# Optimization experiments

Hardware: AMD Instinct MI355X
Metric: run time of the kernel (lower is better)

Reference implementation:

```python
import jax, jax.numpy as jnp
import numpy as np

B = 8192; L = 50; D_EMB = 128
N_USER = 100000; N_MOVIE = 50000; N_DENSE = 8
D = 2 * D_EMB + D_EMB + N_DENSE  # 392 total_input_dim
E = 4; T = 2; H1 = 256; H2 = 128; ATT_H = 64; N_CROSS = 3


def setup_inputs() -> dict:
    key = jax.random.key(0)
    ks = jax.random.split(key, 28)
    rn = lambda k, shape, s=0.02: jax.random.normal(k, shape, jnp.float32) * s
    inp = {
        'userId': jax.random.randint(ks[0], (B,), 0, N_USER),
        'movieId': jax.random.randint(ks[1], (B,), 0, N_MOVIE),
        'seq_history': jax.random.randint(ks[2], (B, L), 0, N_MOVIE),
        'dense_feats': jax.random.normal(ks[3], (B, N_DENSE), jnp.float32),
        # embeddings (row 0 is padding_idx -> zeros)
        'emb_user': rn(ks[4], (N_USER + 1, D_EMB)).at[0].set(0.0),
        'emb_movie': rn(ks[5], (N_MOVIE + 1, D_EMB)).at[0].set(0.0),
        # DIN attention MLP: input [q,k,q-k,q*k] = 4*D_EMB
        'att_w1': rn(ks[6], (4 * D_EMB, ATT_H)), 'att_b1': jnp.zeros((ATT_H,), jnp.float32),
        'att_w2': rn(ks[7], (ATT_H, 1)), 'att_b2': jnp.zeros((1,), jnp.float32),
        # LayerNorms
        'in_gamma': jnp.ones((D,), jnp.float32), 'in_beta': jnp.zeros((D,), jnp.float32),
        'cr_gamma': jnp.ones((D,), jnp.float32), 'cr_beta': jnp.zeros((D,), jnp.float32),
        # CrossNetV2: x_{l+1} = x0 * (x_l W_l + b_l) + x_l
        'cross_W': rn(ks[8], (N_CROSS, D, D)), 'cross_b': jnp.zeros((N_CROSS, D), jnp.float32),
        # MMoE experts: Linear(D,H1)-ReLU-Linear(H1,H2), batched over E
        'exp_w1': rn(ks[9], (E, D, H1)), 'exp_b1': jnp.zeros((E, H1), jnp.float32),
        'exp_w2': rn(ks[10], (E, H1, H2)), 'exp_b2': jnp.zeros((E, H2), jnp.float32),
        # gates per task
        'gate_w': rn(ks[11], (T, D, E)), 'gate_b': jnp.zeros((T, E), jnp.float32),
        # task heads Linear(H2, 1)
        'head_w': rn(ks[12], (T, H2)), 'head_b': jnp.zeros((T,), jnp.float32),
    }
    return inp


def _layernorm(x, g, b, eps=1e-5):
    m = jnp.mean(x, axis=-1, keepdims=True)
    v = jnp.var(x, axis=-1, keepdims=True)
    return (x - m) * jax.lax.rsqrt(v + eps) * g + b


def _forward(userId, movieId, seq_history, dense_feats, emb_user, emb_movie,
             att_w1, att_b1, att_w2, att_b2, in_gamma, in_beta,
             cross_W, cross_b, cr_gamma, cr_beta,
             exp_w1, exp_b1, exp_w2, exp_b2, gate_w, gate_b, head_w, head_b):
    # sparse embedding gathers
    user_e = emb_user[userId]            # [B, D_EMB]
    movie_e = emb_movie[movieId]         # [B, D_EMB]  (target item)
    hist = emb_movie[seq_history]        # [B, L, D_EMB]
    mask = seq_history > 0               # [B, L]

    # DIN attention pooling
    q = jnp.broadcast_to(movie_e[:, None, :], hist.shape)            # [B, L, D_EMB]
    att_in = jnp.concatenate([q, hist, q - hist, q * hist], axis=-1)  # [B, L, 4*D_EMB]
    scores = (jax.nn.relu(att_in @ att_w1 + att_b1) @ att_w2 + att_b2)[..., 0]  # [B, L]
    scores = jnp.where(mask, scores, -1e9)
    probs = jax.nn.softmax(scores, axis=-1)                           # [B, L]
    interest = jnp.einsum('bl,bld->bd', probs, hist)                  # [B, D_EMB]

    x = jnp.concatenate([user_e, movie_e, interest, dense_feats], axis=-1)  # [B, D]
    x = _layernorm(x, in_gamma, in_beta)

    # CrossNetV2
    x0 = x
    for l in range(N_CROSS):
        x = x0 * (x @ cross_W[l] + cross_b[l]) + x
    x = _layernorm(x, cr_gamma, cr_beta)

    # MMoE: batched expert GEMMs + per-task soft gates
    h = jax.nn.relu(jnp.einsum('bd,edh->ebh', x, exp_w1) + exp_b1[:, None, :])  # [E,B,H1]
    eo = jnp.einsum('ebh,eho->ebo', h, exp_w2) + exp_b2[:, None, :]             # [E,B,H2]
    g = jax.nn.softmax(jnp.einsum('bd,tde->tbe', x, gate_w) + gate_b[:, None, :], axis=-1)  # [T,B,E]
    task_feat = jnp.einsum('tbe,ebo->tbo', g, eo)                                # [T,B,H2]

    logits = jnp.einsum('tbo,to->tb', task_feat, head_w) + head_b[:, None]       # [T,B]
    return logits


def reference(userId, movieId, seq_history, dense_feats, emb_user, emb_movie,
              att_w1, att_b1, att_w2, att_b2, in_gamma, in_beta,
              cross_W, cross_b, cr_gamma, cr_beta,
              exp_w1, exp_b1, exp_w2, exp_b2, gate_w, gate_b, head_w, head_b):
    return _forward(userId, movieId, seq_history, dense_feats, emb_user, emb_movie,
                    att_w1, att_b1, att_w2, att_b2, in_gamma, in_beta,
                    cross_W, cross_b, cr_gamma, cr_beta,
                    exp_w1, exp_b1, exp_w2, exp_b2, gate_w, gate_b, head_w, head_b)
```

## Files before the change

kernel.cpp:

```cpp
#include <hip/hip_runtime.h>
#include <hip/hip_bf16.h>

typedef short short8 __attribute__((ext_vector_type(8)));
typedef short short4v __attribute__((ext_vector_type(4)));
typedef float f32x4 __attribute__((ext_vector_type(4)));

constexpr int BB = 8192;
constexpr int LL = 50;
constexpr int DE = 128;
constexpr int DD = 392;
constexpr int HH1 = 256;
constexpr int HH2 = 128;

__device__ __forceinline__ short f2b(float x) {
    __hip_bfloat16 h = __float2bfloat16(x);
    return __builtin_bit_cast(short, h);
}
__device__ __forceinline__ float b2f(short v) {
    unsigned u = ((unsigned)(unsigned short)v) << 16;
    return __builtin_bit_cast(float, u);
}

__global__ __launch_bounds__(256) void prep_small(
    const float* __restrict__ w1,
    const float* __restrict__ w2, const float* __restrict__ b2,
    const float* __restrict__ head_w,
    short* __restrict__ WqpT, float* __restrict__ WkpFf,
    float* __restrict__ hw2, float* __restrict__ hc)
{
    __shared__ float hw[256];
    const int b = blockIdx.x, t = threadIdx.x;
    if (b < 32) {
        int o = b * 256 + t;
        int h = o >> 7, d = o & 127;
        WqpT[o] = f2b(w1[d * 64 + h] + w1[16384 + d * 64 + h]);
    } else if (b < 64) {
        int o = (b - 32) * 256 + t;
        int e = o & 7, lane = (o >> 3) & 63, nt = (o >> 9) & 3, kt = o >> 11;
        int k = (kt << 5) + ((lane >> 4) << 3) + e;
        int h = (nt << 4) + (lane & 15);
        int base = (o >> 3) << 4;
        WkpFf[base + e]     = w1[(128 + k) * 64 + h] - w1[(256 + k) * 64 + h];
        WkpFf[base + 8 + e] = w1[(384 + k) * 64 + h];
    } else {
        const int e = b - 64;
        hw[t] = head_w[t];
        __syncthreads();
        const float* row = &w2[((long)e * HH1 + t) * HH2];
        float s0 = 0.f, s1 = 0.f;
        #pragma unroll 8
        for (int o = 0; o < 128; o += 4) {
            float4 v = *reinterpret_cast<const float4*>(&row[o]);
            s0 += v.x * hw[o] + v.y * hw[o + 1] + v.z * hw[o + 2] + v.w * hw[o + 3];
            s1 += v.x * hw[128 + o] + v.y * hw[129 + o] + v.z * hw[130 + o] + v.w * hw[131 + o];
        }
        hw2[(((e << 8) + t) << 1) + 0] = s0;
        hw2[(((e << 8) + t) << 1) + 1] = s1;
        if (t < 2) {
            float s = 0.f;
            for (int o = 0; o < 128; ++o) s += b2[e * 128 + o] * hw[t * 128 + o];
            hc[e * 2 + t] = s;
        }
    }
}

constexpr int S0 = 3 * 392 * 392;
constexpr int S1 = 4 * 392 * 256;
constexpr int S2 = (50001 * 128) / 4;
constexpr int S3 = (BB * 128) / 4;

__global__ __launch_bounds__(256) void prep_trans(
    const float* __restrict__ cross_W, const float* __restrict__ exp_w1,
    const float* __restrict__ emb_movie, const int* __restrict__ movieId,
    short* __restrict__ WTc, short* __restrict__ WT1, short* __restrict__ embB,
    short* __restrict__ qb)
{
    int idx = blockIdx.x * 256 + threadIdx.x;
    if (idx < S0) {
        int z = idx / (392 * 392), rr = idx - z * 392 * 392;
        int c = rr / 392, r = rr - c * 392;
        WTc[idx] = f2b(cross_W[(long)z * 153664 + r * 392 + c]);
    } else if (idx < S0 + S1) {
        int j = idx - S0;
        int z = j / 100352, rr = j - z * 100352;
        int c = rr / 392, r = rr - c * 392;
        WT1[j] = f2b(exp_w1[(long)z * 100352 + r * 256 + c]);
    } else if (idx < S0 + S1 + S2) {
        long j = (long)(idx - S0 - S1) << 2;
        float4 v = *reinterpret_cast<const float4*>(&emb_movie[j]);
        short4v o;
        o[0] = f2b(v.x); o[1] = f2b(v.y); o[2] = f2b(v.z); o[3] = f2b(v.w);
        *reinterpret_cast<short4v*>(&embB[j]) = o;
    } else if (idx < S0 + S1 + S2 + S3) {
        int j = idx - S0 - S1 - S2;
        int bb = j >> 5, d0 = (j & 31) << 2;
        float4 v = *reinterpret_cast<const float4*>(
            &emb_movie[(long)movieId[bb] * DE + d0]);
        short4v o;
        o[0] = f2b(v.x); o[1] = f2b(v.y); o[2] = f2b(v.z); o[3] = f2b(v.w);
        *reinterpret_cast<short4v*>(&qb[bb * DE + d0]) = o;
    }
}

__global__ __launch_bounds__(256, 8) void attn_kernel(
    const int* __restrict__ userId, const int* __restrict__ movieId,
    const int* __restrict__ seq, const float* __restrict__ dense,
    const float* __restrict__ emb_user, const float* __restrict__ emb_movie,
    const short* __restrict__ embB,
    const float* __restrict__ qcAll, const float* __restrict__ WkpFf,
    const float* __restrict__ att_w2, const float* __restrict__ att_b2,
    const float* __restrict__ in_gamma, const float* __restrict__ in_beta,
    float* __restrict__ x0f, short* __restrict__ x0b)
{
    __shared__ short hist[64 * 128];
    __shared__ float qs[128];
    __shared__ int   seq_s[64];
    __shared__ float spS[4][64];
    __shared__ float probs[64];
    __shared__ float ibuf[4][128];
    __shared__ float stats[2];

    const int b = blockIdx.x;
    const int t = threadIdx.x;
    const int lane = t & 63;
    const int w = t >> 6;

    if (t < 128) qs[t] = emb_movie[(long)movieId[b] * DE + t];
    if (t < 64)  seq_s[t] = (t < LL) ? seq[b * LL + t] : 0;
    __syncthreads();

    #pragma unroll
    for (int i = 0; i < 4; ++i) {
        const int idx = t + (i << 8);
        const int l = idx >> 4, c = idx & 15;
        short8 hv = *reinterpret_cast<const short8*>(&embB[(long)seq_s[l] * DE + (c << 3)]);
        const int byte = (l << 8) + ((c << 4) ^ ((l & 7) << 4));
        *reinterpret_cast<short8*>(reinterpret_cast<char*>(hist) + byte) = hv;
    }

    const int col = (w << 4) + (lane & 15);
    float ue = (t < 128) ? emb_user[(long)userId[b] * DE + t] : 0.f;
    float dv = (t >= 128 && t < 136) ? dense[b * 8 + (t - 128)] : 0.f;
    const float qc  = qcAll[((long)b << 6) + col];
    const float w2v = att_w2[col];

    short8 bfrag[4];
    #pragma unroll
    for (int kt = 0; kt < 4; ++kt) {
        const float* wkp = &WkpFf[((((kt << 2) + w) << 6) | lane) << 4];
        const int kq = (kt << 5) + ((lane >> 4) << 3);
        #pragma unroll
        for (int j = 0; j < 8; ++j)
            bfrag[kt][j] = f2b(fmaf(qs[kq + j], wkp[8 + j], wkp[j]));
    }
    __syncthreads();

    #pragma unroll
    for (int mt = 0; mt < 4; ++mt) {
        f32x4 acc = {0.f, 0.f, 0.f, 0.f};
        const int row = (mt << 4) + (lane & 15);
        const int rbase = row << 8;
        const int swz = (row & 7) << 4;
        #pragma unroll
        for (int kt = 0; kt < 4; ++kt) {
            const int kbyte = (kt << 6) + ((lane >> 4) << 4);
            short8 a = *reinterpret_cast<const short8*>(
                reinterpret_cast<char*>(hist) + rbase + (kbyte ^ swz));
            acc = __builtin_amdgcn_mfma_f32_16x16x32_bf16(a, bfrag[kt], acc, 0, 0, 0);
        }
        #pragma unroll
        for (int r = 0; r < 4; ++r) {
            float v = fmaxf(acc[r] + qc, 0.f) * w2v;
            v += __shfl_xor(v, 1); v += __shfl_xor(v, 2);
            v += __shfl_xor(v, 4); v += __shfl_xor(v, 8);
            if ((lane & 15) == 0)
                spS[w][(mt << 4) + ((lane >> 4) << 2) + r] = v;
        }
    }
    __syncthreads();

    if (t < 64) {
        float sc = spS[0][t] + spS[1][t] + spS[2][t] + spS[3][t] + att_b2[0];
        float s = (t < LL) ? ((seq_s[t] > 0) ? sc : -1e9f) : -INFINITY;
        float m = s;
        #pragma unroll
        for (int off = 32; off > 0; off >>= 1) m = fmaxf(m, __shfl_xor(m, off));
        float e = (t < LL) ? __expf(s - m) : 0.f;
        float sum = e;
        #pragma unroll
        for (int off = 32; off > 0; off >>= 1) sum += __shfl_xor(sum, off);
        probs[t] = (t < LL) ? (e / sum) : 0.f;
    }
    __syncthreads();

    const int g  = t >> 5;
    const int d0 = (t & 31) << 2;
    float4 ps = make_float4(0.f, 0.f, 0.f, 0.f);
    #pragma unroll
    for (int i = 0; i < 8; ++i) {
        const int l = g + (i << 3);
        const int byte = (l << 8) + ((d0 << 1) ^ ((l & 7) << 4));
        short4v hv = *reinterpret_cast<const short4v*>(
            reinterpret_cast<const char*>(hist) + byte);
        const float p = probs[l];
        ps.x = fmaf(p, b2f(hv[0]), ps.x);
        ps.y = fmaf(p, b2f(hv[1]), ps.y);
        ps.z = fmaf(p, b2f(hv[2]), ps.z);
        ps.w = fmaf(p, b2f(hv[3]), ps.w);
    }
    ps.x += __shfl_xor(ps.x, 32); ps.y += __shfl_xor(ps.y, 32);
    ps.z += __shfl_xor(ps.z, 32); ps.w += __shfl_xor(ps.w, 32);
    if (lane < 32)
        *reinterpret_cast<float4*>(&ibuf[w][lane << 2]) = ps;
    __syncthreads();

    float v0 = (t < 128) ? ue : qs[t - 128];
    float v1 = 0.f;
    if (t < 128)       v1 = ibuf[0][t] + ibuf[1][t] + ibuf[2][t] + ibuf[3][t];
    else if (t < 136)  v1 = dv;

    float s2 = v0 + v1, q2 = v0 * v0 + v1 * v1;
    #pragma unroll
    for (int off = 32; off > 0; off >>= 1) {
        s2 += __shfl_xor(s2, off);
        q2 += __shfl_xor(q2, off);
    }
    if (lane == 0) { spS[0][w] = s2; spS[1][w] = q2; }
    __syncthreads();
    if (t == 0) {
        float S = spS[0][0] + spS[0][1] + spS[0][2] + spS[0][3];
        float Q = spS[1][0] + spS[1][1] + spS[1][2] + spS[1][3];
        float mean = S / (float)DD;
        float var = Q / (float)DD - mean * mean;
        stats[0] = mean;
        stats[1] = rsqrtf(var + 1e-5f);
    }
    __syncthreads();
    const float mean = stats[0], inv = stats[1];
    const long base = (long)b * DD;
    float o0 = (v0 - mean) * inv * in_gamma[t] + in_beta[t];
    x0f[base + t] = o0; x0b[base + t] = f2b(o0);
    if (t < 136) {
        float o1 = (v1 - mean) * inv * in_gamma[256 + t] + in_beta[256 + t];
        x0f[base + 256 + t] = o1; x0b[base + 256 + t] = f2b(o1);
    }
}

template<int MODE, int WF32, int WB16, int NXB, int NZB>
__global__ __launch_bounds__(256) void bgemm(
    const short* __restrict__ A, const short* __restrict__ WT,
    const float* __restrict__ bias,
    float* __restrict__ outF, short* __restrict__ outB,
    const float* __restrict__ x0, const float* __restrict__ xin,
    int M, int N, int K, long aZ, long wZ, long bZ, long oZ)
{
    __shared__ short As[2][64 * 64];
    __shared__ short Bs[2][64 * 64];

    int id = blockIdx.x;
    const int qq = (int)gridDim.x >> 3;
    id = (id & 7) * qq + (id >> 3);
    const int mb  = id / (NXB * NZB);
    const int rem = id - mb * (NXB * NZB);
    const int z   = rem / NXB;
    const int xb  = rem - z * NXB;

    A += (long)z * aZ; WT += (long)z * wZ; bias += (long)z * bZ;
    const long oz = (long)z * oZ;

    const int t = threadIdx.x, w = t >> 6, lane = t & 63;
    const int m0 = mb * 64, n0 = xb * 64;
    const int sm = t >> 3, sk8 = (t & 7) << 3;

    f32x4 acc[4];
    #pragma unroll
    for (int i = 0; i < 4; ++i) {
        #pragma unroll
        for (int r = 0; r < 4; ++r) acc[i][r] = 0.f;
    }

    const int nsteps = (K + 63) >> 6;
    short8 avA[2], bvA[2], avB[2], bvB[2];

    auto loadA = [&](int k0) {
        #pragma unroll
        for (int i = 0; i < 2; ++i) {
            const int r = sm + (i << 5);
            short8 zv = {0, 0, 0, 0, 0, 0, 0, 0};
            avA[i] = zv; bvA[i] = zv;
            if (k0 + sk8 < K) {
                avA[i] = *reinterpret_cast<const short8*>(&A[(long)(m0 + r) * K + k0 + sk8]);
                if (n0 + r < N)
                    bvA[i] = *reinterpret_cast<const short8*>(&WT[(long)(n0 + r) * K + k0 + sk8]);
            }
        }
    };
    auto loadB = [&](int k0) {
        #pragma unroll
        for (int i = 0; i < 2; ++i) {
            const int r = sm + (i << 5);
            short8 zv = {0, 0, 0, 0, 0, 0, 0, 0};
            avB[i] = zv; bvB[i] = zv;
            if (k0 + sk8 < K) {
                avB[i] = *reinterpret_cast<const short8*>(&A[(long)(m0 + r) * K + k0 + sk8]);
                if (n0 + r < N)
                    bvB[i] = *reinterpret_cast<const short8*>(&WT[(long)(n0 + r) * K + k0 + sk8]);
            }
        }
    };
    auto wrA = [&](int buf) {
        #pragma unroll
        for (int i = 0; i < 2; ++i) {
            const int r = sm + (i << 5);
            const int byte = (r << 7) + ((sk8 << 1) ^ ((r & 7) << 4));
            *reinterpret_cast<short8*>(reinterpret_cast<char*>(&As[buf][0]) + byte) = avA[i];
            *reinterpret_cast<short8*>(reinterpret_cast<char*>(&Bs[buf][0]) + byte) = bvA[i];
        }
    };
    auto wrB = [&](int buf) {
        #pragma unroll
        for (int i = 0; i < 2; ++i) {
            const int r = sm + (i << 5);
            const int byte = (r << 7) + ((sk8 << 1) ^ ((r & 7) << 4));
            *reinterpret_cast<short8*>(reinterpret_cast<char*>(&As[buf][0]) + byte) = avB[i];
            *reinterpret_cast<short8*>(reinterpret_cast<char*>(&Bs[buf][0]) + byte) = bvB[i];
        }
    };
    auto domfma = [&](int buf) {
        #pragma unroll
        for (int kt = 0; kt < 2; ++kt) {
            const int kbyte = (kt << 6) + ((lane >> 4) << 4);
            const int ar = (w << 4) + (lane & 15);
            short8 a = *reinterpret_cast<const short8*>(
                reinterpret_cast<char*>(&As[buf][0]) + (ar << 7) + (kbyte ^ ((ar & 7) << 4)));
            #pragma unroll
            for (int nt = 0; nt < 4; ++nt) {
                const int br = (nt << 4) + (lane & 15);
                short8 bb = *reinterpret_cast<const short8*>(
                    reinterpret_cast<char*>(&Bs[buf][0]) + (br << 7) + (kbyte ^ ((br & 7) << 4)));
                acc[nt] = __builtin_amdgcn_mfma_f32_16x16x32_bf16(a, bb, acc[nt], 0, 0, 0);
            }
        }
    };

    loadA(0);
    wrA(0);
    if (nsteps > 1) loadA(64);
    if (nsteps > 2) loadB(128);
    __syncthreads();

    int cur = 0, s = 0;
    while (s + 1 < nsteps) {
        domfma(cur);
        wrA(cur ^ 1);
        if (s + 3 < nsteps) loadA((s + 3) << 6);
        __syncthreads(); cur ^= 1; ++s;
        if (s + 1 < nsteps) {
            domfma(cur);
            wrB(cur ^ 1);
            if (s + 3 < nsteps) loadB((s + 3) << 6);
            __syncthreads(); cur ^= 1; ++s;
        }
    }
    domfma(cur);

    #pragma unroll
    for (int nt = 0; nt < 4; ++nt) {
        const int col = n0 + (nt << 4) + (lane & 15);
        if (col < N) {
            const float bv = bias[col];
            #pragma unroll
            for (int r = 0; r < 4; ++r) {
                const int row = m0 + (w << 4) + ((lane >> 4) << 2) + r;
                float v = acc[nt][r] + bv;
                if (MODE == 1) v = fmaxf(v, 0.f);
                const long o = (long)row * N + col;
                if (MODE == 2) v = x0[o] * v + xin[o];
                if (WF32) outF[oz + o] = v;
                if (WB16) outB[oz + o] = f2b(v);
            }
        }
    }
}

__global__ __launch_bounds__(256) void ln_kernel(
    const float* __restrict__ in,
    const float* __restrict__ gamma, const float* __restrict__ beta,
    float* __restrict__ outF, short* __restrict__ outB)
{
    __shared__ float red[2][4];
    __shared__ float stats[2];
    const int b = blockIdx.x, t = threadIdx.x, lane = t & 63, w = t >> 6;
    const long base = (long)b * DD;
    float v0 = in[base + t];
    float v1 = (t < 136) ? in[base + 256 + t] : 0.f;
    float s = v0 + v1, q2 = v0 * v0 + v1 * v1;
    #pragma unroll
    for (int off = 32; off > 0; off >>= 1) {
        s += __shfl_xor(s, off);
        q2 += __shfl_xor(q2, off);
    }
    if (lane == 0) { red[0][w] = s; red[1][w] = q2; }
    __syncthreads();
    if (t == 0) {
        float S = red[0][0] + red[0][1] + red[0][2] + red[0][3];
        float Q = red[1][0] + red[1][1] + red[1][2] + red[1][3];
        float mean = S / (float)DD;
        float var = Q / (float)DD - mean * mean;
        stats[0] = mean;
        stats[1] = rsqrtf(var + 1e-5f);
    }
    __syncthreads();
    const float mean = stats[0], inv = stats[1];
    float o0 = (v0 - mean) * inv * gamma[t] + beta[t];
    outF[base + t] = o0; outB[base + t] = f2b(o0);
    if (t < 136) {
        float o1 = (v1 - mean) * inv * gamma[256 + t] + beta[256 + t];
        outF[base + 256 + t] = o1; outB[base + 256 + t] = f2b(o1);
    }
}

__global__ __launch_bounds__(256) void final_kernel(
    const float* __restrict__ x, const short* __restrict__ h1,
    const float* __restrict__ hw2, const float* __restrict__ hc,
    const float* __restrict__ gate_w, const float* __restrict__ gate_b,
    const float* __restrict__ head_b, float* __restrict__ out)
{
    const int t = threadIdx.x, lane = t & 63, w = t >> 6;
    const int b = blockIdx.x * 4 + w;
    const float* xr = x + (long)b * DD;

    float xv[7];
    #pragma unroll
    for (int i = 0; i < 7; ++i) {
        int d = lane + (i << 6);
        xv[i] = (d < DD) ? xr[d] : 0.f;
    }

    float gl[8] = {0.f, 0.f, 0.f, 0.f, 0.f, 0.f, 0.f, 0.f};
    #pragma unroll
    for (int i = 0; i < 7; ++i) {
        int d = lane + (i << 6);
        if (d < DD) {
            float4 g0 = *reinterpret_cast<const float4*>(&gate_w[d << 2]);
            float4 g1 = *reinterpret_cast<const float4*>(&gate_w[1568 + (d << 2)]);
            gl[0] = fmaf(xv[i], g0.x, gl[0]); gl[1] = fmaf(xv[i], g0.y, gl[1]);
            gl[2] = fmaf(xv[i], g0.z, gl[2]); gl[3] = fmaf(xv[i], g0.w, gl[3]);
            gl[4] = fmaf(xv[i], g1.x, gl[4]); gl[5] = fmaf(xv[i], g1.y, gl[5]);
            gl[6] = fmaf(xv[i], g1.z, gl[6]); gl[7] = fmaf(xv[i], g1.w, gl[7]);
        }
    }

    float ed[8];
    #pragma unroll
    for (int e = 0; e < 4; ++e) {
        short4v hv = *reinterpret_cast<const short4v*>(
            &h1[((long)e * BB + b) * HH1 + (lane << 2)]);
        const float* hwp = &hw2[(((e << 8) + (lane << 2))) << 1];
        float4 w01 = *reinterpret_cast<const float4*>(hwp);
        float4 w23 = *reinterpret_cast<const float4*>(hwp + 4);
        float h0 = b2f(hv[0]), h1f = b2f(hv[1]), h2 = b2f(hv[2]), h3 = b2f(hv[3]);
        ed[e]     = fmaf(h0, w01.x, fmaf(h1f, w01.z, fmaf(h2, w23.x, h3 * w23.z)));
        ed[4 + e] = fmaf(h0, w01.y, fmaf(h1f, w01.w, fmaf(h2, w23.y, h3 * w23.w)));
    }

    #pragma unroll
    for (int v = 0; v < 8; ++v) {
        #pragma unroll
        for (int off = 32; off > 0; off >>= 1) {
            gl[v] += __shfl_xor(gl[v], off);
            ed[v] += __shfl_xor(ed[v], off);
        }
    }

    if (lane == 0) {
        float res[2];
        #pragma unroll
        for (int tt = 0; tt < 2; ++tt) {
            float lv[4], m = -1e30f;
            #pragma unroll
            for (int e = 0; e < 4; ++e) {
                lv[e] = gl[tt * 4 + e] + gate_b[tt * 4 + e];
                m = fmaxf(m, lv[e]);
            }
            float sum = 0.f, acc = 0.f;
            #pragma unroll
            for (int e = 0; e < 4; ++e) { lv[e] = __expf(lv[e] - m); sum += lv[e]; }
            #pragma unroll
            for (int e = 0; e < 4; ++e)
                acc = fmaf(lv[e], ed[tt * 4 + e] + hc[e * 2 + tt], acc);
            res[tt] = head_b[tt] + acc / sum;
        }
        out[b] = res[0];
        out[BB + b] = res[1];
    }
}

extern "C" void kernel_launch(void* const* d_in, const int* in_sizes, int n_in,
                              void* d_out, int out_size, void* d_ws, size_t ws_size,
                              hipStream_t stream) {
    const int*   userId    = (const int*)d_in[0];
    const int*   movieId   = (const int*)d_in[1];
    const int*   seq       = (const int*)d_in[2];
    const float* dense     = (const float*)d_in[3];
    const float* emb_user  = (const float*)d_in[4];
    const float* emb_movie = (const float*)d_in[5];
    const float* att_w1    = (const float*)d_in[6];
    const float* att_b1    = (const float*)d_in[7];
    const float* att_w2    = (const float*)d_in[8];
    const float* att_b2    = (const float*)d_in[9];
    const float* in_gamma  = (const float*)d_in[10];
    const float* in_beta   = (const float*)d_in[11];
    const float* cr_gamma  = (const float*)d_in[12];
    const float* cr_beta   = (const float*)d_in[13];
    const float* cross_W   = (const float*)d_in[14];
    const float* cross_b   = (const float*)d_in[15];
    const float* exp_w1    = (const float*)d_in[16];
    const float* exp_b1    = (const float*)d_in[17];
    const float* exp_w2    = (const float*)d_in[18];
    const float* exp_b2    = (const float*)d_in[19];
    const float* gate_w    = (const float*)d_in[20];
    const float* gate_b    = (const float*)d_in[21];
    const float* head_w    = (const float*)d_in[22];
    const float* head_b    = (const float*)d_in[23];
    float* outp = (float*)d_out;

    char* p = (char*)d_ws;
    auto alloc = [&](size_t bytes) -> char* {
        char* r = p; p += (bytes + 255) & ~(size_t)255; return r;
    };
    short* WqpT  = (short*)alloc(8192 * 2);
    float* WkpFf = (float*)alloc(16384 * 4);
    float* hw2 = (float*)alloc(2048 * 4);
    float* hc  = (float*)alloc(8 * 4);
    short* WTc = (short*)alloc((size_t)3 * 392 * 392 * 2);
    short* WT1 = (short*)alloc((size_t)4 * 256 * 392 * 2);
    short* embB = (short*)alloc((size_t)50001 * 128 * 2);
    short* qb   = (short*)alloc((size_t)BB * DE * 2);
    float* qcAll = (float*)alloc((size_t)BB * 64 * 4);
    float* x0f = (float*)alloc((size_t)BB * DD * 4);
    short* x0b = (short*)alloc((size_t)BB * DD * 2);
    float* xAf = (float*)alloc((size_t)BB * DD * 4);
    short* xAb = (short*)alloc((size_t)BB * DD * 2);
    float* xBf = (float*)alloc((size_t)BB * DD * 4);
    short* xBb = (short*)alloc((size_t)BB * DD * 2);
    short* h1b = (short*)alloc((size_t)4 * BB * HH1 * 2);

    prep_small<<<68, 256, 0, stream>>>(att_w1, exp_w2, exp_b2, head_w,
                                       WqpT, WkpFf, hw2, hc);
    prep_trans<<<(S0 + S1 + S2 + S3 + 255) / 256, 256, 0, stream>>>(
        cross_W, exp_w1, emb_movie, movieId, WTc, WT1, embB, qb);

    bgemm<0, 1, 0, 1, 1><<<128, 256, 0, stream>>>(
        qb, WqpT, att_b1, qcAll, nullptr, nullptr, nullptr,
        BB, 64, DE, 0, 0, 0, 0);

    attn_kernel<<<BB, 256, 0, stream>>>(userId, movieId, seq, dense,
                                        emb_user, emb_movie, embB,
                                        qcAll, WkpFf,
                                        att_w2, att_b2,
                                        in_gamma, in_beta, x0f, x0b);

    bgemm<2, 1, 1, 7, 1><<<896, 256, 0, stream>>>(x0b, WTc, cross_b, xAf, xAb,
                                                  x0f, x0f, BB, DD, DD, 0, 0, 0, 0);
    bgemm<2, 1, 1, 7, 1><<<896, 256, 0, stream>>>(xAb, WTc + 392 * 392, cross_b + 392,
                                                  xBf, xBb, x0f, xAf, BB, DD, DD, 0, 0, 0, 0);
    bgemm<2, 1, 0, 7, 1><<<896, 256, 0, stream>>>(xBb, WTc + 2 * 392 * 392, cross_b + 784,
                                                  xAf, nullptr, x0f, xBf, BB, DD, DD, 0, 0, 0, 0);

    ln_kernel<<<BB, 256, 0, stream>>>(xAf, cr_gamma, cr_beta, xBf, xBb);

    bgemm<1, 0, 1, 4, 4><<<2048, 256, 0, stream>>>(
        xBb, WT1, exp_b1, nullptr, h1b, nullptr, nullptr,
        BB, HH1, DD, 0, (long)HH1 * DD, HH1, (long)BB * HH1);

    final_kernel<<<BB / 4, 256, 0, stream>>>(xBf, h1b, hw2, hc,
                                             gate_w, gate_b, head_b, outp);

    (void)in_sizes; (void)n_in; (void)out_size; (void)ws_size;
}
```

Before: 177.2 us.

## Merge prep kernels, compute query projection inline, simplify GEMM pipeline, drop fp32 LN output

Folds the two prep kernels and the small query-projection GEMM into one prep_all launch, which computes qcAll directly from emb_movie rows with scalar FMAs. This removes two launches and the qb and WqpT intermediates. The GEMM main loop goes from a two-deep register prefetch to a single-buffer prefetch, which cuts register pressure but may hide less load latency. The layernorm now writes only bf16, and the final kernel reads bf16 x for the gate logits, which halves traffic there at some cost in precision.

```diff
diff --git a/kernel.cpp b/kernel.cpp
--- a/kernel.cpp
+++ b/kernel.cpp
@@ -21,29 +21,37 @@
     return __builtin_bit_cast(float, u);
 }
 
-__global__ __launch_bounds__(256) void prep_small(
+constexpr int S0 = 3 * 392 * 392;
+constexpr int S1 = 4 * 392 * 256;
+constexpr int S2 = (50001 * 128) / 4;
+constexpr int NB_TRANS = 9619;
+constexpr int QC0 = 36 + NB_TRANS;
+constexpr int NB_PREP = QC0 + 2048;
+
+__global__ __launch_bounds__(256) void prep_all(
     const float* __restrict__ w1,
     const float* __restrict__ w2, const float* __restrict__ b2,
-    const float* __restrict__ head_w,
-    short* __restrict__ WqpT, float* __restrict__ WkpFf,
-    float* __restrict__ hw2, float* __restrict__ hc)
+    const float* __restrict__ head_w, const float* __restrict__ att_b1,
+    const float* __restrict__ cross_W, const float* __restrict__ exp_w1,
+    const float* __restrict__ emb_movie, const int* __restrict__ movieId,
+    float* __restrict__ WkpFf, float* __restrict__ hw2, float* __restrict__ hc,
+    short* __restrict__ WTc, short* __restrict__ WT1, short* __restrict__ embB,
+    float* __restrict__ qcAll)
 {
-    __shared__ float hw[256];
-    const int b = blockIdx.x, t = threadIdx.x;
-    if (b < 32) {
-        int o = b * 256 + t;
-        int h = o >> 7, d = o & 127;
-        WqpT[o] = f2b(w1[d * 64 + h] + w1[16384 + d * 64 + h]);
-    } else if (b < 64) {
-        int o = (b - 32) * 256 + t;
+    __shared__ float sh[4][128];
+    const int blk = blockIdx.x, t = threadIdx.x;
+
+    if (blk < 32) {
+        int o = blk * 256 + t;
         int e = o & 7, lane = (o >> 3) & 63, nt = (o >> 9) & 3, kt = o >> 11;
         int k = (kt << 5) + ((lane >> 4) << 3) + e;
         int h = (nt << 4) + (lane & 15);
         int base = (o >> 3) << 4;
         WkpFf[base + e]     = w1[(128 + k) * 64 + h] - w1[(256 + k) * 64 + h];
         WkpFf[base + 8 + e] = w1[(384 + k) * 64 + h];
-    } else {
-        const int e = b - 64;
+    } else if (blk < 36) {
+        const int e = blk - 32;
+        float* hw = &sh[0][0];
         hw[t] = head_w[t];
         __syncthreads();
         const float* row = &w2[((long)e * HH1 + t) * HH2];
@@ -61,44 +69,37 @@
             for (int o = 0; o < 128; ++o) s += b2[e * 128 + o] * hw[t * 128 + o];
             hc[e * 2 + t] = s;
         }
-    }
-}
-
-constexpr int S0 = 3 * 392 * 392;
-constexpr int S1 = 4 * 392 * 256;
-constexpr int S2 = (50001 * 128) / 4;
-constexpr int S3 = (BB * 128) / 4;
-
-__global__ __launch_bounds__(256) void prep_trans(
-    const float* __restrict__ cross_W, const float* __restrict__ exp_w1,
-    const float* __restrict__ emb_movie, const int* __restrict__ movieId,
-    short* __restrict__ WTc, short* __restrict__ WT1, short* __restrict__ embB,
-    short* __restrict__ qb)
-{
-    int idx = blockIdx.x * 256 + threadIdx.x;
-    if (idx < S0) {
-        int z = idx / (392 * 392), rr = idx - z * 392 * 392;
-        int c = rr / 392, r = rr - c * 392;
-        WTc[idx] = f2b(cross_W[(long)z * 153664 + r * 392 + c]);
-    } else if (idx < S0 + S1) {
-        int j = idx - S0;
-        int z = j / 100352, rr = j - z * 100352;
-        int c = rr / 392, r = rr - c * 392;
-        WT1[j] = f2b(exp_w1[(long)z * 100352 + r * 256 + c]);
-    } else if (idx < S0 + S1 + S2) {
-        long j = (long)(idx - S0 - S1) << 2;
-        float4 v = *reinterpret_cast<const float4*>(&emb_movie[j]);
-        short4v o;
-        o[0] = f2b(v.x); o[1] = f2b(v.y); o[2] = f2b(v.z); o[3] = f2b(v.w);
-        *reinterpret_cast<short4v*>(&embB[j]) = o;
-    } else if (idx < S0 + S1 + S2 + S3) {
-        int j = idx - S0 - S1 - S2;
-        int bb = j >> 5, d0 = (j & 31) << 2;
-        float4 v = *reinterpret_cast<const float4*>(
-            &emb_movie[(long)movieId[bb] * DE + d0]);
-        short4v o;
-        o[0] = f2b(v.x); o[1] = f2b(v.y); o[2] = f2b(v.z); o[3] = f2b(v.w);
-        *reinterpret_cast<short4v*>(&qb[bb * DE + d0]) = o;
+    } else if (blk < QC0) {
+        int idx = (blk - 36) * 256 + t;
+        if (idx < S0) {
+            int z = idx / (392 * 392), rr = idx - z * 392 * 392;
+            int c = rr / 392, r = rr - c * 392;
+            WTc[idx] = f2b(cross_W[(long)z * 153664 + r * 392 + c]);
+        } else if (idx < S0 + S1) {
+            int j = idx - S0;
+            int z = j / 100352, rr = j - z * 100352;
+            int c = rr / 392, r = rr - c * 392;
+            WT1[j] = f2b(exp_w1[(long)z * 100352 + r * 256 + c]);
+        } else if (idx < S0 + S1 + S2) {
+            long j = (long)(idx - S0 - S1) << 2;
+            float4 v = *reinterpret_cast<const float4*>(&emb_movie[j]);
+            short4v o;
+            o[0] = f2b(v.x); o[1] = f2b(v.y); o[2] = f2b(v.z); o[3] = f2b(v.w);
+            *reinterpret_cast<short4v*>(&embB[j]) = o;
+        }
+    } else {
+        const int w = t >> 6, lane = t & 63;
+        const int b = (blk - QC0) * 4 + w;
+        if (lane < 32)
+            *reinterpret_cast<float4*>(&sh[w][lane << 2]) =
+                *reinterpret_cast<const float4*>(
+                    &emb_movie[(long)movieId[b] * DE + (lane << 2)]);
+        __syncthreads();
+        float s = att_b1[lane];
+        #pragma unroll 8
+        for (int d = 0; d < 128; ++d)
+            s = fmaf(sh[w][d], w1[d * 64 + lane] + w1[16384 + d * 64 + lane], s);
+        qcAll[((long)b << 6) + lane] = s;
     }
 }
 
@@ -211,7 +212,7 @@
     ps.x += __shfl_xor(ps.x, 32); ps.y += __shfl_xor(ps.y, 32);
     ps.z += __shfl_xor(ps.z, 32); ps.w += __shfl_xor(ps.w, 32);
     if (lane < 32)
-        *reinterpret_cast<float4*>(&ibuf[w][lane << 2]) = ps;
+        *reinterpret_cast<float4*>(&ibuf[w][(lane & 31) << 2]) = ps;
     __syncthreads();
 
     float v0 = (t < 128) ? ue : qs[t - 128];
@@ -280,7 +281,7 @@
     }
 
     const int nsteps = (K + 63) >> 6;
-    short8 avA[2], bvA[2], avB[2], bvB[2];
+    short8 avA[2], bvA[2];
 
     auto loadA = [&](int k0) {
         #pragma unroll
@@ -295,19 +296,6 @@
             }
         }
     };
-    auto loadB = [&](int k0) {
-        #pragma unroll
-        for (int i = 0; i < 2; ++i) {
-            const int r = sm + (i << 5);
-            short8 zv = {0, 0, 0, 0, 0, 0, 0, 0};
-            avB[i] = zv; bvB[i] = zv;
-            if (k0 + sk8 < K) {
-                avB[i] = *reinterpret_cast<const short8*>(&A[(long)(m0 + r) * K + k0 + sk8]);
-                if (n0 + r < N)
-                    bvB[i] = *reinterpret_cast<const short8*>(&WT[(long)(n0 + r) * K + k0 + sk8]);
-            }
-        }
-    };
     auto wrA = [&](int buf) {
         #pragma unroll
         for (int i = 0; i < 2; ++i) {
@@ -315,15 +303,6 @@
             const int byte = (r << 7) + ((sk8 << 1) ^ ((r & 7) << 4));
             *reinterpret_cast<short8*>(reinterpret_cast<char*>(&As[buf][0]) + byte) = avA[i];
             *reinterpret_cast<short8*>(reinterpret_cast<char*>(&Bs[buf][0]) + byte) = bvA[i];
-        }
-    };
-    auto wrB = [&](int buf) {
-        #pragma unroll
-        for (int i = 0; i < 2; ++i) {
-            const int r = sm + (i << 5);
-            const int byte = (r << 7) + ((sk8 << 1) ^ ((r & 7) << 4));
-            *reinterpret_cast<short8*>(reinterpret_cast<char*>(&As[buf][0]) + byte) = avB[i];
-            *reinterpret_cast<short8*>(reinterpret_cast<char*>(&Bs[buf][0]) + byte) = bvB[i];
         }
     };
     auto domfma = [&](int buf) {
@@ -346,21 +325,15 @@
     loadA(0);
     wrA(0);
     if (nsteps > 1) loadA(64);
-    if (nsteps > 2) loadB(128);
-    __syncthreads();
-
-    int cur = 0, s = 0;
-    while (s + 1 < nsteps) {
+    __syncthreads();
+
+    int cur = 0;
+    for (int s = 0; s + 1 < nsteps; ++s) {
         domfma(cur);
         wrA(cur ^ 1);
-        if (s + 3 < nsteps) loadA((s + 3) << 6);
-        __syncthreads(); cur ^= 1; ++s;
-        if (s + 1 < nsteps) {
-            domfma(cur);
-            wrB(cur ^ 1);
-            if (s + 3 < nsteps) loadB((s + 3) << 6);
-            __syncthreads(); cur ^= 1; ++s;
-        }
+        if (s + 2 < nsteps) loadA((s + 2) << 6);
+        __syncthreads();
+        cur ^= 1;
     }
     domfma(cur);
 
@@ -386,7 +359,7 @@
 __global__ __launch_bounds__(256) void ln_kernel(
     const float* __restrict__ in,
     const float* __restrict__ gamma, const float* __restrict__ beta,
-    float* __restrict__ outF, short* __restrict__ outB)
+    short* __restrict__ outB)
 {
     __shared__ float red[2][4];
     __shared__ float stats[2];
@@ -412,29 +385,26 @@
     }
     __syncthreads();
     const float mean = stats[0], inv = stats[1];
-    float o0 = (v0 - mean) * inv * gamma[t] + beta[t];
-    outF[base + t] = o0; outB[base + t] = f2b(o0);
-    if (t < 136) {
-        float o1 = (v1 - mean) * inv * gamma[256 + t] + beta[256 + t];
-        outF[base + 256 + t] = o1; outB[base + 256 + t] = f2b(o1);
-    }
+    outB[base + t] = f2b((v0 - mean) * inv * gamma[t] + beta[t]);
+    if (t < 136)
+        outB[base + 256 + t] = f2b((v1 - mean) * inv * gamma[256 + t] + beta[256 + t]);
 }
 
 __global__ __launch_bounds__(256) void final_kernel(
-    const float* __restrict__ x, const short* __restrict__ h1,
+    const short* __restrict__ x, const short* __restrict__ h1,
     const float* __restrict__ hw2, const float* __restrict__ hc,
     const float* __restrict__ gate_w, const float* __restrict__ gate_b,
     const float* __restrict__ head_b, float* __restrict__ out)
 {
     const int t = threadIdx.x, lane = t & 63, w = t >> 6;
     const int b = blockIdx.x * 4 + w;
-    const float* xr = x + (long)b * DD;
+    const short* xr = x + (long)b * DD;
 
     float xv[7];
     #pragma unroll
     for (int i = 0; i < 7; ++i) {
         int d = lane + (i << 6);
-        xv[i] = (d < DD) ? xr[d] : 0.f;
+        xv[i] = (d < DD) ? b2f(xr[d]) : 0.f;
     }
 
     float gl[8] = {0.f, 0.f, 0.f, 0.f, 0.f, 0.f, 0.f, 0.f};
@@ -529,14 +499,12 @@
     auto alloc = [&](size_t bytes) -> char* {
         char* r = p; p += (bytes + 255) & ~(size_t)255; return r;
     };
-    short* WqpT  = (short*)alloc(8192 * 2);
     float* WkpFf = (float*)alloc(16384 * 4);
     float* hw2 = (float*)alloc(2048 * 4);
     float* hc  = (float*)alloc(8 * 4);
     short* WTc = (short*)alloc((size_t)3 * 392 * 392 * 2);
     short* WT1 = (short*)alloc((size_t)4 * 256 * 392 * 2);
     short* embB = (short*)alloc((size_t)50001 * 128 * 2);
-    short* qb   = (short*)alloc((size_t)BB * DE * 2);
     float* qcAll = (float*)alloc((size_t)BB * 64 * 4);
     float* x0f = (float*)alloc((size_t)BB * DD * 4);
     short* x0b = (short*)alloc((size_t)BB * DD * 2);
@@ -544,21 +512,17 @@
     short* xAb = (short*)alloc((size_t)BB * DD * 2);
     float* xBf = (float*)alloc((size_t)BB * DD * 4);
     short* xBb = (short*)alloc((size_t)BB * DD * 2);
+    float* xCf = (float*)alloc((size_t)BB * DD * 4);
+    short* xDb = (short*)alloc((size_t)BB * DD * 2);
     short* h1b = (short*)alloc((size_t)4 * BB * HH1 * 2);
 
-    prep_small<<<68, 256, 0, stream>>>(att_w1, exp_w2, exp_b2, head_w,
-                                       WqpT, WkpFf, hw2, hc);
-    prep_trans<<<(S0 + S1 + S2 + S3 + 255) / 256, 256, 0, stream>>>(
-        cross_W, exp_w1, emb_movie, movieId, WTc, WT1, embB, qb);
-
-    bgemm<0, 1, 0, 1, 1><<<128, 256, 0, stream>>>(
-        qb, WqpT, att_b1, qcAll, nullptr, nullptr, nullptr,
-        BB, 64, DE, 0, 0, 0, 0);
+    prep_all<<<NB_PREP, 256, 0, stream>>>(
+        att_w1, exp_w2, exp_b2, head_w, att_b1, cross_W, exp_w1,
+        emb_movie, movieId, WkpFf, hw2, hc, WTc, WT1, embB, qcAll);
 
     attn_kernel<<<BB, 256, 0, stream>>>(userId, movieId, seq, dense,
                                         emb_user, emb_movie, embB,
-                                        qcAll, WkpFf,
-                                        att_w2, att_b2,
+                                        qcAll, WkpFf, att_w2, att_b2,
                                         in_gamma, in_beta, x0f, x0b);
 
     bgemm<2, 1, 1, 7, 1><<<896, 256, 0, stream>>>(x0b, WTc, cross_b, xAf, xAb,
@@ -566,15 +530,15 @@
     bgemm<2, 1, 1, 7, 1><<<896, 256, 0, stream>>>(xAb, WTc + 392 * 392, cross_b + 392,
                                                   xBf, xBb, x0f, xAf, BB, DD, DD, 0, 0, 0, 0);
     bgemm<2, 1, 0, 7, 1><<<896, 256, 0, stream>>>(xBb, WTc + 2 * 392 * 392, cross_b + 784,
-                                                  xAf, nullptr, x0f, xBf, BB, DD, DD, 0, 0, 0, 0);
-
-    ln_kernel<<<BB, 256, 0, stream>>>(xAf, cr_gamma, cr_beta, xBf, xBb);
+                                                  xCf, nullptr, x0f, xBf, BB, DD, DD, 0, 0, 0, 0);
+
+    ln_kernel<<<BB, 256, 0, stream>>>(xCf, cr_gamma, cr_beta, xDb);
 
     bgemm<1, 0, 1, 4, 4><<<2048, 256, 0, stream>>>(
-        xBb, WT1, exp_b1, nullptr, h1b, nullptr, nullptr,
+        xDb, WT1, exp_b1, nullptr, h1b, nullptr, nullptr,
         BB, HH1, DD, 0, (long)HH1 * DD, HH1, (long)BB * HH1);
 
-    final_kernel<<<BB / 4, 256, 0, stream>>>(xBf, h1b, hw2, hc,
+    final_kernel<<<BB / 4, 256, 0, stream>>>(xDb, h1b, hw2, hc,
                                              gate_w, gate_b, head_b, outp);
 
     (void)in_sizes; (void)n_in; (void)out_size; (void)ws_size;
```

After: 177.3 us. No clear change (+0.0%).
